# Kernel optimization log

Hardware: AMD Instinct MI355X
Metric: run time of the kernel (lower is better)

The kernel has to match this reference:

```python
import jax, jax.numpy as jnp
import numpy as np

MAX_HOPS = 3


def setup_inputs() -> dict:
    key = jax.random.key(0)
    ks = jax.random.split(key, 6)
    B, M, S = 128, 200, 20
    V, D = 100000, 128
    NC, CL = 10000, 10
    stories = jax.random.randint(ks[0], (B, M, S), 0, V, dtype=jnp.int64)
    queries = jax.random.randint(ks[1], (B, S), 0, V, dtype=jnp.int64)
    candidates = jax.random.randint(ks[2], (NC, CL), 0, V, dtype=jnp.int64)
    # 0.05 scale keeps hop softmax logits in a sane range
    A_tab = jax.random.normal(ks[3], (V, D), dtype=jnp.float32) * 0.05
    W_tab = jax.random.normal(ks[4], (V, D), dtype=jnp.float32) * 0.05
    H_w = jax.random.normal(ks[5], (D, D), dtype=jnp.float32) * 0.05
    return {"stories": stories, "queries": queries, "candidates": candidates,
            "A_tab": A_tab, "W_tab": W_tab, "H_w": H_w}


def reference(stories, queries, candidates, A_tab, W_tab, H_w):
    # padding_idx=0: embedding row 0 is zero
    A = A_tab.at[0].set(0.0)
    W = W_tab.at[0].set(0.0)
    # query encoding: gather + sum-pool -> [B, D]
    u = jnp.sum(A[queries], axis=1)
    # memory encoding: [B, M, D] (same A table each hop, as in the source)
    m = jnp.sum(A[stories], axis=2)
    for _ in range(MAX_HOPS):
        dotted = jnp.einsum('bmd,bd->bm', m, u)          # attention logits
        probs = jax.nn.softmax(dotted, axis=1)           # [B, M]
        o = jnp.einsum('bm,bmd->bd', probs, m)           # weighted memory sum
        u = jnp.tanh(u @ H_w.T + o)                      # Linear(no bias) + tanh
    cand_sum = jnp.sum(W[candidates], axis=1)            # [NC, D]
    logits = u @ cand_sum.T                              # [B, NC]
    return logits
```

## Files before the change

kernel.cpp:

```cpp
#include <hip/hip_runtime.h>
#include <hip/hip_bf16.h>
#include <math.h>

#define BB 128
#define MM 200
#define SS 20
#define DD 128
#define NC 10000
#define CL 10
#define LCT 64

__device__ __forceinline__ unsigned pack_bf16(float a, float b) {
    unsigned ua = __float_as_uint(a), ub = __float_as_uint(b);
    ua += 0x7fff + ((ua >> 16) & 1);
    ub += 0x7fff + ((ub >> 16) & 1);
    return (ua >> 16) | (ub & 0xffff0000u);
}
__device__ __forceinline__ float bflo(unsigned v) { return __uint_as_float(v << 16); }
__device__ __forceinline__ float bfhi(unsigned v) { return __uint_as_float(v & 0xffff0000u); }

__device__ __forceinline__ int detect_shift(const int* __restrict__ q) {
    int zc = 0;
#pragma unroll
    for (int i = 0; i < 8; ++i) zc += (q[2 * i + 1] == 0);
    return (zc >= 6) ? 1 : 0;
}

__global__ __launch_bounds__(512) void k_conv(const float* __restrict__ A,
                                              unsigned* __restrict__ Abf) {
    size_t t = (size_t)blockIdx.x * 512 + threadIdx.x;
    const float4* in = (const float4*)(A + t * 8);
    float4 a = in[0], b = in[1];
    if (t * 8 < DD) {
        a = make_float4(0.f, 0.f, 0.f, 0.f);
        b = make_float4(0.f, 0.f, 0.f, 0.f);
    }
    uint4 o;
    o.x = pack_bf16(a.x, a.y);
    o.y = pack_bf16(a.z, a.w);
    o.z = pack_bf16(b.x, b.y);
    o.w = pack_bf16(b.z, b.w);
    ((uint4*)(Abf + t * 4))[0] = o;
}

__global__ __launch_bounds__(512) void k_main(const int* __restrict__ stories,
                                              const int* __restrict__ queries,
                                              const int* __restrict__ cands,
                                              const unsigned* __restrict__ Abf,
                                              const float* __restrict__ W,
                                              const float* __restrict__ Hw,
                                              float* __restrict__ uT,
                                              float* __restrict__ cand_buf) {
    __shared__ unsigned m_s[MM][DD / 2];
    __shared__ float u_s[DD];
    __shared__ float p_s[MM];
    __shared__ float o_part[8][DD];
    __shared__ float red_s;

    int bid = blockIdx.x;
    int tid = threadIdx.x;
    int shift = detect_shift(queries);

    if (bid < BB) {
        int b = bid;
        int g = tid >> 4, l = tid & 15;
#pragma unroll
        for (int r = 0; r < 7; ++r) {
            int mm = g + (r << 5);
            if (mm < MM) {
                int toks[SS];
#pragma unroll
                for (int s = 0; s < SS; ++s)
                    toks[s] = stories[((size_t)((b * MM + mm) * SS + s)) << shift];
                float a[8] = {0.f, 0.f, 0.f, 0.f, 0.f, 0.f, 0.f, 0.f};
#pragma unroll
                for (int s = 0; s < SS; ++s) {
                    uint4 v = ((const uint4*)(Abf + (size_t)toks[s] * (DD / 2)))[l];
                    a[0] += bflo(v.x); a[1] += bfhi(v.x);
                    a[2] += bflo(v.y); a[3] += bfhi(v.y);
                    a[4] += bflo(v.z); a[5] += bfhi(v.z);
                    a[6] += bflo(v.w); a[7] += bfhi(v.w);
                }
                uint4 o;
                o.x = pack_bf16(a[0], a[1]);
                o.y = pack_bf16(a[2], a[3]);
                o.z = pack_bf16(a[4], a[5]);
                o.w = pack_bf16(a[6], a[7]);
                *(uint4*)&m_s[mm][4 * l] = o;
            }
        }
        if (tid < DD) {
            int d = tid;
            float acc = 0.f;
#pragma unroll
            for (int s = 0; s < SS; ++s) {
                int tok = queries[((size_t)(b * SS + s)) << shift];
                unsigned pv = Abf[(size_t)tok * (DD / 2) + (d >> 1)];
                acc += (d & 1) ? bfhi(pv) : bflo(pv);
            }
            u_s[d] = acc;
        }
        __syncthreads();

        for (int hop = 0; hop < 3; ++hop) {
            if (tid < MM) {
                const float2* u2 = (const float2*)u_s;
                float acc = 0.f;
#pragma unroll 8
                for (int li = 0; li < 64; ++li) {
                    int j = (tid + li) & 63;
                    unsigned pv = m_s[tid][j];
                    float2 uv = u2[j];
                    acc += bflo(pv) * uv.x + bfhi(pv) * uv.y;
                }
                p_s[tid] = acc;
            }
            __syncthreads();
            if (tid < 64) {
                float v0 = p_s[tid], v1 = p_s[tid + 64], v2 = p_s[tid + 128];
                float v3 = (tid < 8) ? p_s[tid + 192] : -1e30f;
                float mx = fmaxf(fmaxf(v0, v1), fmaxf(v2, v3));
                for (int off = 32; off; off >>= 1) mx = fmaxf(mx, __shfl_down(mx, off));
                mx = __shfl(mx, 0);
                float e0 = __expf(v0 - mx), e1 = __expf(v1 - mx), e2 = __expf(v2 - mx);
                float e3 = (tid < 8) ? __expf(v3 - mx) : 0.f;
                float sm = e0 + e1 + e2 + e3;
                for (int off = 32; off; off >>= 1) sm += __shfl_down(sm, off);
                p_s[tid] = e0;
                p_s[tid + 64] = e1;
                p_s[tid + 128] = e2;
                if (tid < 8) p_s[tid + 192] = e3;
                if (tid == 0) red_s = 1.f / __shfl(sm, 0);
            }
            __syncthreads();
            {
                int c = tid & 63, h = tid >> 6;
                int mm0 = h * 25;
                float ax = 0.f, ay = 0.f;
#pragma unroll 5
                for (int k = 0; k < 25; ++k) {
                    unsigned pv = m_s[mm0 + k][c];
                    float p = p_s[mm0 + k];
                    ax = fmaf(p, bflo(pv), ax);
                    ay = fmaf(p, bfhi(pv), ay);
                }
                o_part[h][2 * c] = ax;
                o_part[h][2 * c + 1] = ay;
            }
            __syncthreads();
            float u_new = 0.f;
            if (tid < DD) {
                float o = 0.f;
#pragma unroll
                for (int h = 0; h < 8; ++h) o += o_part[h][tid];
                float acc = o * red_s;
                const float4* hrow = (const float4*)(Hw + tid * DD);
                const float4* u4 = (const float4*)u_s;
#pragma unroll 8
                for (int j = 0; j < DD / 4; ++j) {
                    float4 hv = hrow[j];
                    float4 uv = u4[j];
                    acc += hv.x * uv.x + hv.y * uv.y + hv.z * uv.z + hv.w * uv.w;
                }
                u_new = tanhf(acc);
            }
            __syncthreads();
            if (tid < DD) u_s[tid] = u_new;
            __syncthreads();
        }
        if (tid < DD) uT[tid * BB + bid] = u_s[tid];
    } else {
        int g = tid >> 5, l = tid & 31;
        int row = (bid - BB) * 16 + g;
        int toks[CL];
#pragma unroll
        for (int s = 0; s < CL; ++s)
            toks[s] = cands[((size_t)(row * CL + s)) << shift];
        float4 acc = make_float4(0.f, 0.f, 0.f, 0.f);
#pragma unroll
        for (int s = 0; s < CL; ++s) {
            float4 v = ((const float4*)(W + (size_t)toks[s] * DD))[l];
            float msk = toks[s] ? 1.f : 0.f;
            acc.x = fmaf(msk, v.x, acc.x);
            acc.y = fmaf(msk, v.y, acc.y);
            acc.z = fmaf(msk, v.z, acc.z);
            acc.w = fmaf(msk, v.w, acc.w);
        }
        ((float4*)(cand_buf + (size_t)row * DD))[l] = acc;
    }
}

__global__ __launch_bounds__(256) void k_logits(const float* __restrict__ uT,
                                                const float* __restrict__ cs,
                                                float* __restrict__ out) {
    __shared__ float c_s[DD][LCT + 4];
    int c0 = blockIdx.x * LCT;
    int tid = threadIdx.x;
    {
        int c = tid >> 2, l = tid & 3;
        int row = c0 + c;
        if (row >= NC) row = NC - 1;
        const float4* rp = (const float4*)(cs + (size_t)row * DD);
#pragma unroll
        for (int i = 0; i < 8; ++i) {
            int k = (l << 5) + (i << 2);
            float4 v = rp[(l << 3) + i];
            c_s[k][c] = v.x;
            c_s[k + 1][c] = v.y;
            c_s[k + 2][c] = v.z;
            c_s[k + 3][c] = v.w;
        }
    }
    __syncthreads();
    int tx = tid & 31, ty = tid >> 5;
    const float* cb = &c_s[0][ty << 3];
    const float4* up = (const float4*)(uT + (tx << 2));
    float acc[4][8];
#pragma unroll
    for (int i = 0; i < 4; ++i)
#pragma unroll
        for (int j = 0; j < 8; ++j) acc[i][j] = 0.f;
#pragma unroll 4
    for (int k = 0; k < DD; ++k) {
        float4 uv = up[k * (BB / 4)];
        float4 ca = *(const float4*)(cb + k * (LCT + 4));
        float4 cc = *(const float4*)(cb + k * (LCT + 4) + 4);
        float uu[4] = {uv.x, uv.y, uv.z, uv.w};
        float cv[8] = {ca.x, ca.y, ca.z, ca.w, cc.x, cc.y, cc.z, cc.w};
#pragma unroll
        for (int i = 0; i < 4; ++i)
#pragma unroll
            for (int j = 0; j < 8; ++j) acc[i][j] = fmaf(uu[i], cv[j], acc[i][j]);
    }
    if (c0 + (ty << 3) < NC) {
#pragma unroll
        for (int i = 0; i < 4; ++i) {
            float* orow = out + (size_t)((tx << 2) + i) * NC + c0 + (ty << 3);
            ((float4*)orow)[0] = make_float4(acc[i][0], acc[i][1], acc[i][2], acc[i][3]);
            ((float4*)orow)[1] = make_float4(acc[i][4], acc[i][5], acc[i][6], acc[i][7]);
        }
    }
}

extern "C" void kernel_launch(void* const* d_in, const int* in_sizes, int n_in,
                              void* d_out, int out_size, void* d_ws, size_t ws_size,
                              hipStream_t stream) {
    const int* stories = (const int*)d_in[0];
    const int* queries = (const int*)d_in[1];
    const int* cands   = (const int*)d_in[2];
    const float* A  = (const float*)d_in[3];
    const float* W  = (const float*)d_in[4];
    const float* Hw = (const float*)d_in[5];
    float* out = (float*)d_out;

    unsigned* Abf = (unsigned*)d_ws;
    float* cand_buf = (float*)(Abf + 100000 * (DD / 2));
    float* uT_buf = cand_buf + (size_t)NC * DD;

    k_conv<<<100000 * DD / 8 / 512, 512, 0, stream>>>(A, Abf);
    k_main<<<BB + NC / 16, 512, 0, stream>>>(stories, queries, cands, Abf, W, Hw,
                                             uT_buf, cand_buf);
    k_logits<<<(NC + LCT - 1) / LCT, 256, 0, stream>>>(uT_buf, cand_buf, out);
}
```

Baseline: 184.5 us.

## Split story gather into a widely parallel kernel separate from hop computation

The story/query/candidate embedding gathers move out of the per-batch hop kernel into a dedicated gather kernel with 1600+ blocks. Before, only 128 blocks did all the story gathering, which left most of the GPU idle. The gathered memory is written to global memory in bf16, and a new 128-block hop kernel copies it back into LDS. This costs an extra kernel launch and roughly 6.5 MB of round-trip global traffic.

```diff
diff --git a/kernel.cpp b/kernel.cpp
--- a/kernel.cpp
+++ b/kernel.cpp
@@ -9,6 +9,10 @@
 #define NC 10000
 #define CL 10
 #define LCT 64
+#define NROW (BB * MM)
+#define GS_BLK (NROW / 16)
+#define GQ_BLK (BB / 16)
+#define GC_BLK (NC / 8)
 
 __device__ __forceinline__ unsigned pack_bf16(float a, float b) {
     unsigned ua = __float_as_uint(a), ub = __float_as_uint(b);
@@ -43,151 +47,168 @@
     ((uint4*)(Abf + t * 4))[0] = o;
 }
 
-__global__ __launch_bounds__(512) void k_main(const int* __restrict__ stories,
-                                              const int* __restrict__ queries,
-                                              const int* __restrict__ cands,
-                                              const unsigned* __restrict__ Abf,
-                                              const float* __restrict__ W,
+__global__ __launch_bounds__(256) void k_gather(const int* __restrict__ stories,
+                                                const int* __restrict__ queries,
+                                                const int* __restrict__ cands,
+                                                const unsigned* __restrict__ Abf,
+                                                const float* __restrict__ W,
+                                                unsigned* __restrict__ m_all,
+                                                float* __restrict__ u0_all,
+                                                float* __restrict__ cand_buf) {
+    int bid = blockIdx.x;
+    int tid = threadIdx.x;
+    int shift = detect_shift(queries);
+
+    if (bid < GS_BLK) {
+        int g = tid >> 4, l = tid & 15;
+        int r = bid * 16 + g;
+        int toks[SS];
+#pragma unroll
+        for (int s = 0; s < SS; ++s)
+            toks[s] = stories[((size_t)(r * SS + s)) << shift];
+        float a[8] = {0.f, 0.f, 0.f, 0.f, 0.f, 0.f, 0.f, 0.f};
+#pragma unroll
+        for (int s = 0; s < SS; ++s) {
+            uint4 v = ((const uint4*)(Abf + ((size_t)(unsigned)toks[s] << 6)))[l];
+            a[0] += bflo(v.x); a[1] += bfhi(v.x);
+            a[2] += bflo(v.y); a[3] += bfhi(v.y);
+            a[4] += bflo(v.z); a[5] += bfhi(v.z);
+            a[6] += bflo(v.w); a[7] += bfhi(v.w);
+        }
+        uint4 o;
+        o.x = pack_bf16(a[0], a[1]);
+        o.y = pack_bf16(a[2], a[3]);
+        o.z = pack_bf16(a[4], a[5]);
+        o.w = pack_bf16(a[6], a[7]);
+        ((uint4*)(m_all + (size_t)r * (DD / 2)))[l] = o;
+    } else if (bid < GS_BLK + GQ_BLK) {
+        int g = tid >> 4, l = tid & 15;
+        int b = (bid - GS_BLK) * 16 + g;
+        int toks[SS];
+#pragma unroll
+        for (int s = 0; s < SS; ++s)
+            toks[s] = queries[((size_t)(b * SS + s)) << shift];
+        float a[8] = {0.f, 0.f, 0.f, 0.f, 0.f, 0.f, 0.f, 0.f};
+#pragma unroll
+        for (int s = 0; s < SS; ++s) {
+            uint4 v = ((const uint4*)(Abf + ((size_t)(unsigned)toks[s] << 6)))[l];
+            a[0] += bflo(v.x); a[1] += bfhi(v.x);
+            a[2] += bflo(v.y); a[3] += bfhi(v.y);
+            a[4] += bflo(v.z); a[5] += bfhi(v.z);
+            a[6] += bflo(v.w); a[7] += bfhi(v.w);
+        }
+        float4* op = (float4*)(u0_all + (size_t)b * DD + l * 8);
+        op[0] = make_float4(a[0], a[1], a[2], a[3]);
+        op[1] = make_float4(a[4], a[5], a[6], a[7]);
+    } else {
+        int g = tid >> 5, l = tid & 31;
+        int row = (bid - GS_BLK - GQ_BLK) * 8 + g;
+        int toks[CL];
+#pragma unroll
+        for (int s = 0; s < CL; ++s)
+            toks[s] = cands[((size_t)(row * CL + s)) << shift];
+        float4 acc = make_float4(0.f, 0.f, 0.f, 0.f);
+#pragma unroll
+        for (int s = 0; s < CL; ++s) {
+            float4 v = ((const float4*)(W + (size_t)(unsigned)toks[s] * DD))[l];
+            float msk = toks[s] ? 1.f : 0.f;
+            acc.x = fmaf(msk, v.x, acc.x);
+            acc.y = fmaf(msk, v.y, acc.y);
+            acc.z = fmaf(msk, v.z, acc.z);
+            acc.w = fmaf(msk, v.w, acc.w);
+        }
+        ((float4*)(cand_buf + (size_t)row * DD))[l] = acc;
+    }
+}
+
+__global__ __launch_bounds__(512) void k_hops(const unsigned* __restrict__ m_all,
+                                              const float* __restrict__ u0_all,
                                               const float* __restrict__ Hw,
-                                              float* __restrict__ uT,
-                                              float* __restrict__ cand_buf) {
+                                              float* __restrict__ uT) {
     __shared__ unsigned m_s[MM][DD / 2];
     __shared__ float u_s[DD];
     __shared__ float p_s[MM];
     __shared__ float o_part[8][DD];
     __shared__ float red_s;
 
-    int bid = blockIdx.x;
+    int b = blockIdx.x;
     int tid = threadIdx.x;
-    int shift = detect_shift(queries);
-
-    if (bid < BB) {
-        int b = bid;
-        int g = tid >> 4, l = tid & 15;
-#pragma unroll
-        for (int r = 0; r < 7; ++r) {
-            int mm = g + (r << 5);
-            if (mm < MM) {
-                int toks[SS];
-#pragma unroll
-                for (int s = 0; s < SS; ++s)
-                    toks[s] = stories[((size_t)((b * MM + mm) * SS + s)) << shift];
-                float a[8] = {0.f, 0.f, 0.f, 0.f, 0.f, 0.f, 0.f, 0.f};
-#pragma unroll
-                for (int s = 0; s < SS; ++s) {
-                    uint4 v = ((const uint4*)(Abf + (size_t)toks[s] * (DD / 2)))[l];
-                    a[0] += bflo(v.x); a[1] += bfhi(v.x);
-                    a[2] += bflo(v.y); a[3] += bfhi(v.y);
-                    a[4] += bflo(v.z); a[5] += bfhi(v.z);
-                    a[6] += bflo(v.w); a[7] += bfhi(v.w);
-                }
-                uint4 o;
-                o.x = pack_bf16(a[0], a[1]);
-                o.y = pack_bf16(a[2], a[3]);
-                o.z = pack_bf16(a[4], a[5]);
-                o.w = pack_bf16(a[6], a[7]);
-                *(uint4*)&m_s[mm][4 * l] = o;
+
+    {
+        const uint4* src = (const uint4*)(m_all + (size_t)b * MM * (DD / 2));
+        uint4* dst = (uint4*)&m_s[0][0];
+        for (int i = tid; i < MM * (DD / 2) / 4; i += 512) dst[i] = src[i];
+    }
+    if (tid < DD) u_s[tid] = u0_all[(size_t)b * DD + tid];
+    __syncthreads();
+
+    for (int hop = 0; hop < 3; ++hop) {
+        if (tid < MM) {
+            const float2* u2 = (const float2*)u_s;
+            float acc = 0.f;
+#pragma unroll 8
+            for (int li = 0; li < 64; ++li) {
+                int j = (tid + li) & 63;
+                unsigned pv = m_s[tid][j];
+                float2 uv = u2[j];
+                acc += bflo(pv) * uv.x + bfhi(pv) * uv.y;
             }
-        }
+            p_s[tid] = acc;
+        }
+        __syncthreads();
+        if (tid < 64) {
+            float v0 = p_s[tid], v1 = p_s[tid + 64], v2 = p_s[tid + 128];
+            float v3 = (tid < 8) ? p_s[tid + 192] : -1e30f;
+            float mx = fmaxf(fmaxf(v0, v1), fmaxf(v2, v3));
+            for (int off = 32; off; off >>= 1) mx = fmaxf(mx, __shfl_down(mx, off));
+            mx = __shfl(mx, 0);
+            float e0 = __expf(v0 - mx), e1 = __expf(v1 - mx), e2 = __expf(v2 - mx);
+            float e3 = (tid < 8) ? __expf(v3 - mx) : 0.f;
+            float sm = e0 + e1 + e2 + e3;
+            for (int off = 32; off; off >>= 1) sm += __shfl_down(sm, off);
+            p_s[tid] = e0;
+            p_s[tid + 64] = e1;
+            p_s[tid + 128] = e2;
+            if (tid < 8) p_s[tid + 192] = e3;
+            if (tid == 0) red_s = 1.f / __shfl(sm, 0);
+        }
+        __syncthreads();
+        {
+            int c = tid & 63, h = tid >> 6;
+            int mm0 = h * 25;
+            float ax = 0.f, ay = 0.f;
+#pragma unroll 5
+            for (int k = 0; k < 25; ++k) {
+                unsigned pv = m_s[mm0 + k][c];
+                float p = p_s[mm0 + k];
+                ax = fmaf(p, bflo(pv), ax);
+                ay = fmaf(p, bfhi(pv), ay);
+            }
+            o_part[h][2 * c] = ax;
+            o_part[h][2 * c + 1] = ay;
+        }
+        __syncthreads();
+        float u_new = 0.f;
         if (tid < DD) {
-            int d = tid;
-            float acc = 0.f;
-#pragma unroll
-            for (int s = 0; s < SS; ++s) {
-                int tok = queries[((size_t)(b * SS + s)) << shift];
-                unsigned pv = Abf[(size_t)tok * (DD / 2) + (d >> 1)];
-                acc += (d & 1) ? bfhi(pv) : bflo(pv);
+            float o = 0.f;
+#pragma unroll
+            for (int h = 0; h < 8; ++h) o += o_part[h][tid];
+            float acc = o * red_s;
+            const float4* hrow = (const float4*)(Hw + tid * DD);
+            const float4* u4 = (const float4*)u_s;
+#pragma unroll 8
+            for (int j = 0; j < DD / 4; ++j) {
+                float4 hv = hrow[j];
+                float4 uv = u4[j];
+                acc += hv.x * uv.x + hv.y * uv.y + hv.z * uv.z + hv.w * uv.w;
             }
-            u_s[d] = acc;
-        }
-        __syncthreads();
-
-        for (int hop = 0; hop < 3; ++hop) {
-            if (tid < MM) {
-                const float2* u2 = (const float2*)u_s;
-                float acc = 0.f;
-#pragma unroll 8
-                for (int li = 0; li < 64; ++li) {
-                    int j = (tid + li) & 63;
-                    unsigned pv = m_s[tid][j];
-                    float2 uv = u2[j];
-                    acc += bflo(pv) * uv.x + bfhi(pv) * uv.y;
-                }
-                p_s[tid] = acc;
-            }
-            __syncthreads();
-            if (tid < 64) {
-                float v0 = p_s[tid], v1 = p_s[tid + 64], v2 = p_s[tid + 128];
-                float v3 = (tid < 8) ? p_s[tid + 192] : -1e30f;
-                float mx = fmaxf(fmaxf(v0, v1), fmaxf(v2, v3));
-                for (int off = 32; off; off >>= 1) mx = fmaxf(mx, __shfl_down(mx, off));
-                mx = __shfl(mx, 0);
-                float e0 = __expf(v0 - mx), e1 = __expf(v1 - mx), e2 = __expf(v2 - mx);
-                float e3 = (tid < 8) ? __expf(v3 - mx) : 0.f;
-                float sm = e0 + e1 + e2 + e3;
-                for (int off = 32; off; off >>= 1) sm += __shfl_down(sm, off);
-                p_s[tid] = e0;
-                p_s[tid + 64] = e1;
-                p_s[tid + 128] = e2;
-                if (tid < 8) p_s[tid + 192] = e3;
-                if (tid == 0) red_s = 1.f / __shfl(sm, 0);
-            }
-            __syncthreads();
-            {
-                int c = tid & 63, h = tid >> 6;
-                int mm0 = h * 25;
-                float ax = 0.f, ay = 0.f;
-#pragma unroll 5
-                for (int k = 0; k < 25; ++k) {
-                    unsigned pv = m_s[mm0 + k][c];
-                    float p = p_s[mm0 + k];
-                    ax = fmaf(p, bflo(pv), ax);
-                    ay = fmaf(p, bfhi(pv), ay);
-                }
-                o_part[h][2 * c] = ax;
-                o_part[h][2 * c + 1] = ay;
-            }
-            __syncthreads();
-            float u_new = 0.f;
-            if (tid < DD) {
-                float o = 0.f;
-#pragma unroll
-                for (int h = 0; h < 8; ++h) o += o_part[h][tid];
-                float acc = o * red_s;
-                const float4* hrow = (const float4*)(Hw + tid * DD);
-                const float4* u4 = (const float4*)u_s;
-#pragma unroll 8
-                for (int j = 0; j < DD / 4; ++j) {
-                    float4 hv = hrow[j];
-                    float4 uv = u4[j];
-                    acc += hv.x * uv.x + hv.y * uv.y + hv.z * uv.z + hv.w * uv.w;
-                }
-                u_new = tanhf(acc);
-            }
-            __syncthreads();
-            if (tid < DD) u_s[tid] = u_new;
-            __syncthreads();
-        }
-        if (tid < DD) uT[tid * BB + bid] = u_s[tid];
-    } else {
-        int g = tid >> 5, l = tid & 31;
-        int row = (bid - BB) * 16 + g;
-        int toks[CL];
-#pragma unroll
-        for (int s = 0; s < CL; ++s)
-            toks[s] = cands[((size_t)(row * CL + s)) << shift];
-        float4 acc = make_float4(0.f, 0.f, 0.f, 0.f);
-#pragma unroll
-        for (int s = 0; s < CL; ++s) {
-            float4 v = ((const float4*)(W + (size_t)toks[s] * DD))[l];
-            float msk = toks[s] ? 1.f : 0.f;
-            acc.x = fmaf(msk, v.x, acc.x);
-            acc.y = fmaf(msk, v.y, acc.y);
-            acc.z = fmaf(msk, v.z, acc.z);
-            acc.w = fmaf(msk, v.w, acc.w);
-        }
-        ((float4*)(cand_buf + (size_t)row * DD))[l] = acc;
-    }
+            u_new = tanhf(acc);
+        }
+        __syncthreads();
+        if (tid < DD) u_s[tid] = u_new;
+        __syncthreads();
+    }
+    if (tid < DD) uT[tid * BB + b] = u_s[tid];
 }
 
 __global__ __launch_bounds__(256) void k_logits(const float* __restrict__ uT,
@@ -254,11 +275,15 @@
     float* out = (float*)d_out;
 
     unsigned* Abf = (unsigned*)d_ws;
-    float* cand_buf = (float*)(Abf + 100000 * (DD / 2));
+    float* cand_buf = (float*)(Abf + (size_t)100000 * (DD / 2));
     float* uT_buf = cand_buf + (size_t)NC * DD;
+    float* u0_buf = uT_buf + (size_t)BB * DD;
+    unsigned* m_all = (unsigned*)(u0_buf + (size_t)BB * DD);
 
     k_conv<<<100000 * DD / 8 / 512, 512, 0, stream>>>(A, Abf);
-    k_main<<<BB + NC / 16, 512, 0, stream>>>(stories, queries, cands, Abf, W, Hw,
-                                             uT_buf, cand_buf);
+    k_gather<<<GS_BLK + GQ_BLK + GC_BLK, 256, 0, stream>>>(stories, queries, cands,
+                                                           Abf, W, m_all, u0_buf,
+                                                           cand_buf);
+    k_hops<<<BB, 512, 0, stream>>>(m_all, u0_buf, Hw, uT_buf);
     k_logits<<<(NC + LCT - 1) / LCT, 256, 0, stream>>>(uT_buf, cand_buf, out);
 }
```

New measurement: 189.1 us. +2.5%, slower.
